# Kernel tuning notes

Measured on AMD Instinct MI355X. Metric: run time of the kernel, lower is better.

## Reference

```python
import jax, jax.numpy as jnp
import numpy as np

B, S, D, H = 4, 2048, 1024, 16
DH = D // H


def setup_inputs() -> dict:
    key = jax.random.key(0)
    ks = jax.random.split(key, 12)
    scale = 1.0 / np.sqrt(D)
    inp = {
        'q': jax.random.normal(ks[0], (B, S, D), jnp.float32),
        'k': jax.random.normal(ks[1], (B, S, D), jnp.float32),
        'v': jax.random.normal(ks[2], (B, S, D), jnp.float32),
        # causal mask, broadcast over batch and heads; masked where mask == 0
        'mask': jnp.tril(jnp.ones((S, S), jnp.int32))[None, None, :, :],
        'wq': jax.random.normal(ks[3], (D, D), jnp.float32) * scale,
        'bq': jnp.zeros((D,), jnp.float32),
        'wk': jax.random.normal(ks[4], (D, D), jnp.float32) * scale,
        'bk': jnp.zeros((D,), jnp.float32),
        'wv': jax.random.normal(ks[5], (D, D), jnp.float32) * scale,
        'bv': jnp.zeros((D,), jnp.float32),
        'wo': jax.random.normal(ks[6], (D, D), jnp.float32) * scale,
        'bo': jnp.zeros((D,), jnp.float32),
    }
    return inp


def _split_heads(x):
    # [B, S, D] -> [B, H, S, DH]
    b, s, _ = x.shape
    return x.reshape(b, s, H, DH).transpose(0, 2, 1, 3)


def reference(q, k, v, mask, wq, bq, wk, bk, wv, bv, wo, bo):
    # torch Linear: y = x @ W.T + b
    qh = _split_heads(q @ wq.T + bq)
    kh = _split_heads(k @ wk.T + bk)
    vh = _split_heads(v @ wv.T + bv)
    attn = jnp.einsum('bhqd,bhkd->bhqk', qh, kh) / np.sqrt(DH)
    attn = jnp.where(mask == 0, jnp.float32(-10000.0), attn)
    attn = jax.nn.softmax(attn, axis=-1)
    out = jnp.einsum('bhqk,bhkd->bhqd', attn, vh)
    out = out.transpose(0, 2, 1, 3).reshape(q.shape[0], q.shape[1], D)
    return out @ wo.T + bo
```

## Files before the change

kernel.cpp:

```cpp
#include <hip/hip_runtime.h>

typedef __attribute__((ext_vector_type(8))) short short8;
typedef __attribute__((ext_vector_type(4))) float f32x4;
typedef __attribute__((ext_vector_type(16))) float f32x16;
typedef __attribute__((ext_vector_type(4))) unsigned short ushort4v;
typedef __attribute__((ext_vector_type(8))) unsigned short ushort8v;
typedef __attribute__((ext_vector_type(4))) unsigned int uint4v;

#define S_LEN 2048
#define DMODEL 1024
#define NHEAD 16
#define DHEAD 64
#define BATCH 4
#define NEGBIG (-1.0e30f)
#define LOG2E 1.4426950408889634f

__device__ __forceinline__ unsigned short f2bf(float f) {
  unsigned int u = __builtin_bit_cast(unsigned int, f);
  u += 0x7fffu + ((u >> 16) & 1u);
  return (unsigned short)(u >> 16);
}

__device__ __forceinline__ void gload16(const void* src, void* lds_dst) {
  __builtin_amdgcn_global_load_lds(
      (const __attribute__((address_space(1))) unsigned int*)src,
      (__attribute__((address_space(3))) unsigned int*)lds_dst, 16, 0, 0);
}

__global__ __launch_bounds__(256) void cvt3_kernel(
    const float* __restrict__ i0, const float* __restrict__ i1, const float* __restrict__ i2,
    unsigned short* __restrict__ o0, unsigned short* __restrict__ o1,
    unsigned short* __restrict__ o2, int n) {
  const float* in = (blockIdx.y == 0) ? i0 : (blockIdx.y == 1) ? i1 : i2;
  unsigned short* out = (blockIdx.y == 0) ? o0 : (blockIdx.y == 1) ? o1 : o2;
  int idx = blockIdx.x * blockDim.x + threadIdx.x;
  int stride = gridDim.x * blockDim.x;
  for (int j = idx * 8; j < n; j += stride * 8) {
    float4 a = *(const float4*)(in + j);
    float4 b = *(const float4*)(in + j + 4);
    ushort8v r;
    r[0] = f2bf(a.x); r[1] = f2bf(a.y); r[2] = f2bf(a.z); r[3] = f2bf(a.w);
    r[4] = f2bf(b.x); r[5] = f2bf(b.y); r[6] = f2bf(b.z); r[7] = f2bf(b.w);
    *(ushort8v*)(out + j) = r;
  }
}

__global__ __launch_bounds__(256) void cvt4_kernel(
    const float* __restrict__ i0, const float* __restrict__ i1,
    const float* __restrict__ i2, const float* __restrict__ i3,
    unsigned short* __restrict__ o0, unsigned short* __restrict__ o1,
    unsigned short* __restrict__ o2, unsigned short* __restrict__ o3, int n) {
  const float* in = (blockIdx.y == 0) ? i0 : (blockIdx.y == 1) ? i1 : (blockIdx.y == 2) ? i2 : i3;
  unsigned short* out = (blockIdx.y == 0) ? o0 : (blockIdx.y == 1) ? o1 : (blockIdx.y == 2) ? o2 : o3;
  int idx = blockIdx.x * blockDim.x + threadIdx.x;
  int stride = gridDim.x * blockDim.x;
  for (int j = idx * 8; j < n; j += stride * 8) {
    float4 a = *(const float4*)(in + j);
    float4 b = *(const float4*)(in + j + 4);
    ushort8v r;
    r[0] = f2bf(a.x); r[1] = f2bf(a.y); r[2] = f2bf(a.z); r[3] = f2bf(a.w);
    r[4] = f2bf(b.x); r[5] = f2bf(b.y); r[6] = f2bf(b.z); r[7] = f2bf(b.w);
    *(ushort8v*)(out + j) = r;
  }
}

template <int MODE>
__global__ __launch_bounds__(256) void gemm_kernel(
    const unsigned short* __restrict__ A, const unsigned short* __restrict__ W,
    const float* __restrict__ bias, void* __restrict__ outp, int M, int N, int K,
    float oscale) {
  __shared__ char lds[32768];
  const int tid = threadIdx.x;
  const int lane = tid & 63;
  const int wv = tid >> 6;
  const int wr = wv >> 1, wc = wv & 1;
  const int l16 = lane & 15, lg = lane >> 4;

  const int nbx = N >> 7;
  const int nwg = gridDim.x;
  const int swz = (blockIdx.x & 7) * (nwg >> 3) + (blockIdx.x >> 3);
  const int tm = swz / nbx, tn = swz % nbx;

  const char* Ab = (const char*)A;
  const char* Wb = (const char*)W;

  f32x4 acc[4][4] = {};

  for (int k0 = 0; k0 < K; k0 += 64) {
#pragma unroll
    for (int i = 0; i < 8; ++i) {
      int ch = wv * 8 + i;
      int chl = ch & 15;
      int r = chl * 8 + (lane >> 3);
      int cb = ((lane & 7) * 16) ^ ((r & 7) << 4);
      const char* src = (ch < 16)
          ? Ab + ((size_t)(tm * 128 + r) * K + k0) * 2 + cb
          : Wb + ((size_t)(tn * 128 + r) * K + k0) * 2 + cb;
      gload16(src, lds + ch * 1024);
    }
    __syncthreads();
#pragma unroll
    for (int ks = 0; ks < 2; ++ks) {
      const int cbase = (ks * 32 + lg * 8) * 2;
      short8 af[4], bfr[4];
#pragma unroll
      for (int m = 0; m < 4; ++m) {
        int r = wr * 64 + m * 16 + l16;
        af[m] = *(const short8*)(lds + r * 128 + (cbase ^ ((r & 7) << 4)));
      }
#pragma unroll
      for (int n = 0; n < 4; ++n) {
        int r = wc * 64 + n * 16 + l16;
        bfr[n] = *(const short8*)(lds + 16384 + r * 128 + (cbase ^ ((r & 7) << 4)));
      }
#pragma unroll
      for (int m = 0; m < 4; ++m)
#pragma unroll
        for (int n = 0; n < 4; ++n)
          acc[m][n] = __builtin_amdgcn_mfma_f32_16x16x32_bf16(af[m], bfr[n], acc[m][n], 0, 0, 0);
    }
    __syncthreads();
  }

#pragma unroll
  for (int n = 0; n < 4; ++n) {
    int gn = tn * 128 + wc * 64 + n * 16 + l16;
    float bv = bias[gn];
#pragma unroll
    for (int m = 0; m < 4; ++m) {
      int gm0 = tm * 128 + wr * 64 + m * 16 + lg * 4;
      f32x4 a = acc[m][n];
      if (MODE == 2) {
        float* of = (float*)outp;
#pragma unroll
        for (int rr = 0; rr < 4; ++rr)
          of[(size_t)(gm0 + rr) * N + gn] = (a[rr] + bv) * oscale;
      } else if (MODE == 0) {
        unsigned short* ou = (unsigned short*)outp;
        int h = gn >> 6, dh = gn & 63;
#pragma unroll
        for (int rr = 0; rr < 4; ++rr) {
          int gm = gm0 + rr;
          int b = gm >> 11, s = gm & 2047;
          ou[(((size_t)b * NHEAD + h) * S_LEN + s) * DHEAD + dh] = f2bf((a[rr] + bv) * oscale);
        }
      } else {
        unsigned short* ou = (unsigned short*)outp;
        int h = gn >> 6, dh = gn & 63;
        int b = gm0 >> 11, s0 = gm0 & 2047;
        ushort4v pk;
        pk[0] = f2bf((a[0] + bv) * oscale); pk[1] = f2bf((a[1] + bv) * oscale);
        pk[2] = f2bf((a[2] + bv) * oscale); pk[3] = f2bf((a[3] + bv) * oscale);
        *(ushort4v*)(ou + (((size_t)b * NHEAD + h) * DHEAD + dh) * S_LEN + s0) = pk;
      }
    }
  }
}

__global__ __launch_bounds__(256) void attn_kernel(
    const unsigned short* __restrict__ qh, const unsigned short* __restrict__ kh,
    const unsigned short* __restrict__ vt, unsigned short* __restrict__ aout) {
  __shared__ char lds[32768];
  const int tid = threadIdx.x;
  const int lane = tid & 63;
  const int w = tid >> 6;
  const int l31 = lane & 31;
  const int l5 = lane >> 5;
  const int bh = blockIdx.y;
  const int b = bh >> 4, h = bh & 15;

  const char* kbase = (const char*)(kh + (size_t)bh * S_LEN * DHEAD);
  const char* vbase = (const char*)(vt + (size_t)bh * S_LEN * DHEAD);
  const unsigned short* qbase = qh + (size_t)bh * S_LEN * DHEAD;

  const int la = lane >> 3, lb = lane & 7;

  for (int ph = 0; ph < 2; ++ph) {
    const int qb = ph ? (15 - (int)blockIdx.x) : (int)blockIdx.x;
    const int q0 = qb * 128;
    const int wq0 = q0 + w * 32;
    const int qg = wq0 + l31;
    const int nt = qb * 2 + 2;

    short8 qf[4];
#pragma unroll
    for (int f = 0; f < 4; ++f)
      qf[f] = *(const short8*)(qbase + (size_t)qg * DHEAD + f * 16 + l5 * 8);

    f32x16 oa[2] = {};
    float mrun = NEGBIG, lr = 0.f;

#pragma unroll
    for (int i = 0; i < 2; ++i) {
      int ch = w * 2 + i;
      int r = ch * 8 + la;
      int cb = (lb * 16) ^ ((r & 7) << 4);
      gload16(kbase + (size_t)r * 128 + cb, lds + ch * 1024 + lane * 16);
      gload16(vbase + (size_t)r * 4096 + cb, lds + 8192 + ch * 1024 + lane * 16);
    }
    __syncthreads();
    int cur = 0;

    for (int t = 0; t < nt; ++t) {
      const int kv0 = t * 64;
      if (t + 1 < nt) {
        char* nb = lds + (cur ^ 1) * 16384;
#pragma unroll
        for (int i = 0; i < 2; ++i) {
          int ch = w * 2 + i;
          int r = ch * 8 + la;
          int cb = (lb * 16) ^ ((r & 7) << 4);
          gload16(kbase + (size_t)(kv0 + 64 + r) * 128 + cb, nb + ch * 1024 + lane * 16);
          gload16(vbase + (size_t)r * 4096 + (size_t)(kv0 + 64) * 2 + cb,
                  nb + 8192 + ch * 1024 + lane * 16);
        }
      }
      if (kv0 <= wq0 + 31) {
        const char* ldk = lds + cur * 16384;
        const char* ldv = ldk + 8192;

        f32x16 sa[2] = {};
#pragma unroll
        for (int kb2 = 0; kb2 < 2; ++kb2) {
          const int kr = kb2 * 32 + l31;
          const char* rowp = ldk + kr * 128;
          const int sw = (kr & 7) << 4;
#pragma unroll
          for (int f = 0; f < 4; ++f) {
            short8 kf = *(const short8*)(rowp + ((f * 32 + l5 * 16) ^ sw));
            sa[kb2] = __builtin_amdgcn_mfma_f32_32x32x16_bf16(kf, qf[f], sa[kb2], 0, 0, 0);
          }
        }

        if (kv0 + 63 > wq0) {
#pragma unroll
          for (int kb2 = 0; kb2 < 2; ++kb2)
#pragma unroll
            for (int r = 0; r < 16; ++r) {
              int kgl = kv0 + kb2 * 32 + (r & 3) + 8 * (r >> 2) + 4 * l5;
              if (kgl > qg) sa[kb2][r] = NEGBIG;
            }
        }

        float pm = sa[0][0];
#pragma unroll
        for (int kb2 = 0; kb2 < 2; ++kb2)
#pragma unroll
          for (int r = 0; r < 16; ++r) pm = fmaxf(pm, sa[kb2][r]);
        pm = fmaxf(pm, __shfl_xor(pm, 32));

        if (!__all(pm <= mrun + 8.f)) {
          float mN = fmaxf(mrun, pm);
          float sc = __builtin_amdgcn_exp2f(mrun - mN);
          mrun = mN;
          lr *= sc;
          oa[0] *= sc;
          oa[1] *= sc;
        }

        float rs = 0.f;
        short8 pfrag[4];
#pragma unroll
        for (int kb2 = 0; kb2 < 2; ++kb2) {
          unsigned int wpk[8];
#pragma unroll
          for (int i = 0; i < 8; ++i) {
            float p0 = __builtin_amdgcn_exp2f(sa[kb2][2 * i] - mrun);
            float p1 = __builtin_amdgcn_exp2f(sa[kb2][2 * i + 1] - mrun);
            rs += p0 + p1;
            wpk[i] = (unsigned int)f2bf(p0) | ((unsigned int)f2bf(p1) << 16);
          }
#pragma unroll
          for (int g = 0; g < 2; ++g) {
            unsigned int o0 = l5 ? wpk[4 * g + 2] : wpk[4 * g];
            unsigned int o1 = l5 ? wpk[4 * g + 3] : wpk[4 * g + 1];
            unsigned int s0 = l5 ? wpk[4 * g] : wpk[4 * g + 2];
            unsigned int s1 = l5 ? wpk[4 * g + 1] : wpk[4 * g + 3];
            unsigned int r0 = (unsigned int)__shfl_xor((int)s0, 32);
            unsigned int r1 = (unsigned int)__shfl_xor((int)s1, 32);
            uint4v fw;
            fw[0] = l5 ? r0 : o0;
            fw[1] = l5 ? r1 : o1;
            fw[2] = l5 ? o0 : r0;
            fw[3] = l5 ? o1 : r1;
            pfrag[kb2 * 2 + g] = __builtin_bit_cast(short8, fw);
          }
        }
        rs += __shfl_xor(rs, 32);
        lr += rs;

#pragma unroll
        for (int db = 0; db < 2; ++db) {
          const int vr = db * 32 + l31;
          const char* rowp = ldv + vr * 128;
          const int sw = (vr & 7) << 4;
#pragma unroll
          for (int f = 0; f < 4; ++f) {
            short8 vf = *(const short8*)(rowp + ((f * 32 + l5 * 16) ^ sw));
            oa[db] = __builtin_amdgcn_mfma_f32_32x32x16_bf16(vf, pfrag[f], oa[db], 0, 0, 0);
          }
        }
      }
      __syncthreads();
      cur ^= 1;
    }

    float rl = 1.0f / lr;
    unsigned short* obase = aout + ((size_t)(b * S_LEN + qg)) * DMODEL + h * DHEAD;
#pragma unroll
    for (int db = 0; db < 2; ++db)
#pragma unroll
      for (int rq = 0; rq < 4; ++rq) {
        ushort4v pk;
#pragma unroll
        for (int j = 0; j < 4; ++j)
          pk[j] = f2bf(oa[db][rq * 4 + j] * rl);
        *(ushort4v*)(obase + db * 32 + 8 * rq + 4 * l5) = pk;
      }
  }
}

extern "C" void kernel_launch(void* const* d_in, const int* in_sizes, int n_in,
                              void* d_out, int out_size, void* d_ws, size_t ws_size,
                              hipStream_t stream) {
  (void)in_sizes; (void)n_in; (void)out_size; (void)ws_size;
  const float* q  = (const float*)d_in[0];
  const float* k  = (const float*)d_in[1];
  const float* v  = (const float*)d_in[2];
  const float* wq = (const float*)d_in[4];
  const float* bq = (const float*)d_in[5];
  const float* wk = (const float*)d_in[6];
  const float* bk = (const float*)d_in[7];
  const float* wv = (const float*)d_in[8];
  const float* bv = (const float*)d_in[9];
  const float* wo = (const float*)d_in[10];
  const float* bo = (const float*)d_in[11];

  const size_t NACT = (size_t)BATCH * S_LEN * DMODEL;
  const size_t NW = (size_t)DMODEL * DMODEL;
  unsigned short* qb  = (unsigned short*)d_ws;
  unsigned short* kb  = qb + NACT;
  unsigned short* vb  = kb + NACT;
  unsigned short* wqb = vb + NACT;
  unsigned short* wkb = wqb + NW;
  unsigned short* wvb = wkb + NW;
  unsigned short* wob = wvb + NW;
  unsigned short* qhb = wob + NW;
  unsigned short* khb = qhb + NACT;
  unsigned short* vtb = khb + NACT;
  unsigned short* aout = qb;

  dim3 blk(256);
  cvt3_kernel<<<dim3(2048, 3), blk, 0, stream>>>(q, k, v, qb, kb, vb, (int)NACT);
  cvt4_kernel<<<dim3(512, 4), blk, 0, stream>>>(wq, wk, wv, wo, wqb, wkb, wvb, wob, (int)NW);

  const int M = BATCH * S_LEN, N = DMODEL, K = DMODEL;
  const int grid = (M / 128) * (N / 128);
  gemm_kernel<0><<<grid, blk, 0, stream>>>(qb, wqb, bq, qhb, M, N, K, 0.125f * LOG2E);
  gemm_kernel<0><<<grid, blk, 0, stream>>>(kb, wkb, bk, khb, M, N, K, 1.0f);
  gemm_kernel<1><<<grid, blk, 0, stream>>>(vb, wvb, bv, vtb, M, N, K, 1.0f);

  attn_kernel<<<dim3(8, 64), blk, 0, stream>>>(qhb, khb, vtb, aout);

  gemm_kernel<2><<<grid, blk, 0, stream>>>(aout, wob, bo, d_out, M, N, K, 1.0f);
}
```

Baseline: 204.3 us.

## Use 512-thread attention blocks covering 256 queries instead of paired 128-query phases

The attention kernel now launches 8 waves per block, each block handling a 256-query tile in a single pass, and drops the two-phase pairing of a short and a long causal tile. Each thread issues one K and one V async load per KV tile, so more waves share each LDS-staged tile. Blocks are ordered with the heaviest query tiles first. This trades the old per-block causal load balancing for better K/V reuse and fewer loop phases, and risks tail imbalance between blocks with very different tile counts.

```diff
diff --git a/kernel.cpp b/kernel.cpp
--- a/kernel.cpp
+++ b/kernel.cpp
@@ -157,7 +157,7 @@
   }
 }
 
-__global__ __launch_bounds__(256) void attn_kernel(
+__global__ __launch_bounds__(512) void attn_kernel(
     const unsigned short* __restrict__ qh, const unsigned short* __restrict__ kh,
     const unsigned short* __restrict__ vt, unsigned short* __restrict__ aout) {
   __shared__ char lds[32768];
@@ -173,151 +173,138 @@
   const char* vbase = (const char*)(vt + (size_t)bh * S_LEN * DHEAD);
   const unsigned short* qbase = qh + (size_t)bh * S_LEN * DHEAD;
 
-  const int la = lane >> 3, lb = lane & 7;
-
-  for (int ph = 0; ph < 2; ++ph) {
-    const int qb = ph ? (15 - (int)blockIdx.x) : (int)blockIdx.x;
-    const int q0 = qb * 128;
-    const int wq0 = q0 + w * 32;
-    const int qg = wq0 + l31;
-    const int nt = qb * 2 + 2;
-
-    short8 qf[4];
-#pragma unroll
-    for (int f = 0; f < 4; ++f)
-      qf[f] = *(const short8*)(qbase + (size_t)qg * DHEAD + f * 16 + l5 * 8);
-
-    f32x16 oa[2] = {};
-    float mrun = NEGBIG, lr = 0.f;
-
-#pragma unroll
-    for (int i = 0; i < 2; ++i) {
-      int ch = w * 2 + i;
-      int r = ch * 8 + la;
-      int cb = (lb * 16) ^ ((r & 7) << 4);
-      gload16(kbase + (size_t)r * 128 + cb, lds + ch * 1024 + lane * 16);
-      gload16(vbase + (size_t)r * 4096 + cb, lds + 8192 + ch * 1024 + lane * 16);
+  const int sr = tid >> 3;
+  const int scb = ((tid & 7) * 16) ^ ((sr & 7) << 4);
+  const int sdst = tid * 16;
+
+  const int qb = 7 - (int)blockIdx.x;
+  const int q0 = qb * 256;
+  const int wq0 = q0 + w * 32;
+  const int qg = wq0 + l31;
+  const int nt = qb * 4 + 4;
+
+  short8 qf[4];
+#pragma unroll
+  for (int f = 0; f < 4; ++f)
+    qf[f] = *(const short8*)(qbase + (size_t)qg * DHEAD + f * 16 + l5 * 8);
+
+  f32x16 oa[2] = {};
+  float mrun = NEGBIG, lr = 0.f;
+
+  gload16(kbase + (size_t)sr * 128 + scb, lds + sdst);
+  gload16(vbase + (size_t)sr * 4096 + scb, lds + 8192 + sdst);
+  __syncthreads();
+  int cur = 0;
+
+  for (int t = 0; t < nt; ++t) {
+    const int kv0 = t * 64;
+    if (t + 1 < nt) {
+      char* nb = lds + (cur ^ 1) * 16384;
+      gload16(kbase + (size_t)(kv0 + 64 + sr) * 128 + scb, nb + sdst);
+      gload16(vbase + (size_t)sr * 4096 + (size_t)(kv0 + 64) * 2 + scb, nb + 8192 + sdst);
+    }
+    if (kv0 <= wq0 + 31) {
+      const char* ldk = lds + cur * 16384;
+      const char* ldv = ldk + 8192;
+
+      f32x16 sa[2] = {};
+#pragma unroll
+      for (int kb2 = 0; kb2 < 2; ++kb2) {
+        const int kr = kb2 * 32 + l31;
+        const char* rowp = ldk + kr * 128;
+        const int sw = (kr & 7) << 4;
+#pragma unroll
+        for (int f = 0; f < 4; ++f) {
+          short8 kf = *(const short8*)(rowp + ((f * 32 + l5 * 16) ^ sw));
+          sa[kb2] = __builtin_amdgcn_mfma_f32_32x32x16_bf16(kf, qf[f], sa[kb2], 0, 0, 0);
+        }
+      }
+
+      if (kv0 + 63 > wq0) {
+#pragma unroll
+        for (int kb2 = 0; kb2 < 2; ++kb2)
+#pragma unroll
+          for (int r = 0; r < 16; ++r) {
+            int kgl = kv0 + kb2 * 32 + (r & 3) + 8 * (r >> 2) + 4 * l5;
+            if (kgl > qg) sa[kb2][r] = NEGBIG;
+          }
+      }
+
+      float pm = sa[0][0];
+#pragma unroll
+      for (int kb2 = 0; kb2 < 2; ++kb2)
+#pragma unroll
+        for (int r = 0; r < 16; ++r) pm = fmaxf(pm, sa[kb2][r]);
+      pm = fmaxf(pm, __shfl_xor(pm, 32));
+
+      if (!__all(pm <= mrun + 8.f)) {
+        float mN = fmaxf(mrun, pm);
+        float sc = __builtin_amdgcn_exp2f(mrun - mN);
+        mrun = mN;
+        lr *= sc;
+        oa[0] *= sc;
+        oa[1] *= sc;
+      }
+
+      float rs = 0.f;
+      short8 pfrag[4];
+#pragma unroll
+      for (int kb2 = 0; kb2 < 2; ++kb2) {
+        unsigned int wpk[8];
+#pragma unroll
+        for (int i = 0; i < 8; ++i) {
+          float p0 = __builtin_amdgcn_exp2f(sa[kb2][2 * i] - mrun);
+          float p1 = __builtin_amdgcn_exp2f(sa[kb2][2 * i + 1] - mrun);
+          rs += p0 + p1;
+          wpk[i] = (unsigned int)f2bf(p0) | ((unsigned int)f2bf(p1) << 16);
+        }
+#pragma unroll
+        for (int g = 0; g < 2; ++g) {
+          unsigned int o0 = l5 ? wpk[4 * g + 2] : wpk[4 * g];
+          unsigned int o1 = l5 ? wpk[4 * g + 3] : wpk[4 * g + 1];
+          unsigned int s0 = l5 ? wpk[4 * g] : wpk[4 * g + 2];
+          unsigned int s1 = l5 ? wpk[4 * g + 1] : wpk[4 * g + 3];
+          unsigned int r0 = (unsigned int)__shfl_xor((int)s0, 32);
+          unsigned int r1 = (unsigned int)__shfl_xor((int)s1, 32);
+          uint4v fw;
+          fw[0] = l5 ? r0 : o0;
+          fw[1] = l5 ? r1 : o1;
+          fw[2] = l5 ? o0 : r0;
+          fw[3] = l5 ? o1 : r1;
+          pfrag[kb2 * 2 + g] = __builtin_bit_cast(short8, fw);
+        }
+      }
+      rs += __shfl_xor(rs, 32);
+      lr += rs;
+
+#pragma unroll
+      for (int db = 0; db < 2; ++db) {
+        const int vr = db * 32 + l31;
+        const char* rowp = ldv + vr * 128;
+        const int sw = (vr & 7) << 4;
+#pragma unroll
+        for (int f = 0; f < 4; ++f) {
+          short8 vf = *(const short8*)(rowp + ((f * 32 + l5 * 16) ^ sw));
+          oa[db] = __builtin_amdgcn_mfma_f32_32x32x16_bf16(vf, pfrag[f], oa[db], 0, 0, 0);
+        }
+      }
     }
     __syncthreads();
-    int cur = 0;
-
-    for (int t = 0; t < nt; ++t) {
-      const int kv0 = t * 64;
-      if (t + 1 < nt) {
-        char* nb = lds + (cur ^ 1) * 16384;
-#pragma unroll
-        for (int i = 0; i < 2; ++i) {
-          int ch = w * 2 + i;
-          int r = ch * 8 + la;
-          int cb = (lb * 16) ^ ((r & 7) << 4);
-          gload16(kbase + (size_t)(kv0 + 64 + r) * 128 + cb, nb + ch * 1024 + lane * 16);
-          gload16(vbase + (size_t)r * 4096 + (size_t)(kv0 + 64) * 2 + cb,
-                  nb + 8192 + ch * 1024 + lane * 16);
-        }
-      }
-      if (kv0 <= wq0 + 31) {
-        const char* ldk = lds + cur * 16384;
-        const char* ldv = ldk + 8192;
-
-        f32x16 sa[2] = {};
-#pragma unroll
-        for (int kb2 = 0; kb2 < 2; ++kb2) {
-          const int kr = kb2 * 32 + l31;
-          const char* rowp = ldk + kr * 128;
-          const int sw = (kr & 7) << 4;
-#pragma unroll
-          for (int f = 0; f < 4; ++f) {
-            short8 kf = *(const short8*)(rowp + ((f * 32 + l5 * 16) ^ sw));
-            sa[kb2] = __builtin_amdgcn_mfma_f32_32x32x16_bf16(kf, qf[f], sa[kb2], 0, 0, 0);
-          }
-        }
-
-        if (kv0 + 63 > wq0) {
-#pragma unroll
-          for (int kb2 = 0; kb2 < 2; ++kb2)
-#pragma unroll
-            for (int r = 0; r < 16; ++r) {
-              int kgl = kv0 + kb2 * 32 + (r & 3) + 8 * (r >> 2) + 4 * l5;
-              if (kgl > qg) sa[kb2][r] = NEGBIG;
-            }
-        }
-
-        float pm = sa[0][0];
-#pragma unroll
-        for (int kb2 = 0; kb2 < 2; ++kb2)
-#pragma unroll
-          for (int r = 0; r < 16; ++r) pm = fmaxf(pm, sa[kb2][r]);
-        pm = fmaxf(pm, __shfl_xor(pm, 32));
-
-        if (!__all(pm <= mrun + 8.f)) {
-          float mN = fmaxf(mrun, pm);
-          float sc = __builtin_amdgcn_exp2f(mrun - mN);
-          mrun = mN;
-          lr *= sc;
-          oa[0] *= sc;
-          oa[1] *= sc;
-        }
-
-        float rs = 0.f;
-        short8 pfrag[4];
-#pragma unroll
-        for (int kb2 = 0; kb2 < 2; ++kb2) {
-          unsigned int wpk[8];
-#pragma unroll
-          for (int i = 0; i < 8; ++i) {
-            float p0 = __builtin_amdgcn_exp2f(sa[kb2][2 * i] - mrun);
-            float p1 = __builtin_amdgcn_exp2f(sa[kb2][2 * i + 1] - mrun);
-            rs += p0 + p1;
-            wpk[i] = (unsigned int)f2bf(p0) | ((unsigned int)f2bf(p1) << 16);
-          }
-#pragma unroll
-          for (int g = 0; g < 2; ++g) {
-            unsigned int o0 = l5 ? wpk[4 * g + 2] : wpk[4 * g];
-            unsigned int o1 = l5 ? wpk[4 * g + 3] : wpk[4 * g + 1];
-            unsigned int s0 = l5 ? wpk[4 * g] : wpk[4 * g + 2];
-            unsigned int s1 = l5 ? wpk[4 * g + 1] : wpk[4 * g + 3];
-            unsigned int r0 = (unsigned int)__shfl_xor((int)s0, 32);
-            unsigned int r1 = (unsigned int)__shfl_xor((int)s1, 32);
-            uint4v fw;
-            fw[0] = l5 ? r0 : o0;
-            fw[1] = l5 ? r1 : o1;
-            fw[2] = l5 ? o0 : r0;
-            fw[3] = l5 ? o1 : r1;
-            pfrag[kb2 * 2 + g] = __builtin_bit_cast(short8, fw);
-          }
-        }
-        rs += __shfl_xor(rs, 32);
-        lr += rs;
-
-#pragma unroll
-        for (int db = 0; db < 2; ++db) {
-          const int vr = db * 32 + l31;
-          const char* rowp = ldv + vr * 128;
-          const int sw = (vr & 7) << 4;
-#pragma unroll
-          for (int f = 0; f < 4; ++f) {
-            short8 vf = *(const short8*)(rowp + ((f * 32 + l5 * 16) ^ sw));
-            oa[db] = __builtin_amdgcn_mfma_f32_32x32x16_bf16(vf, pfrag[f], oa[db], 0, 0, 0);
-          }
-        }
-      }
-      __syncthreads();
-      cur ^= 1;
-    }
-
-    float rl = 1.0f / lr;
-    unsigned short* obase = aout + ((size_t)(b * S_LEN + qg)) * DMODEL + h * DHEAD;
-#pragma unroll
-    for (int db = 0; db < 2; ++db)
-#pragma unroll
-      for (int rq = 0; rq < 4; ++rq) {
-        ushort4v pk;
-#pragma unroll
-        for (int j = 0; j < 4; ++j)
-          pk[j] = f2bf(oa[db][rq * 4 + j] * rl);
-        *(ushort4v*)(obase + db * 32 + 8 * rq + 4 * l5) = pk;
-      }
-  }
+    cur ^= 1;
+  }
+
+  float rl = 1.0f / lr;
+  unsigned short* obase = aout + ((size_t)(b * S_LEN + qg)) * DMODEL + h * DHEAD;
+#pragma unroll
+  for (int db = 0; db < 2; ++db)
+#pragma unroll
+    for (int rq = 0; rq < 4; ++rq) {
+      ushort4v pk;
+#pragma unroll
+      for (int j = 0; j < 4; ++j)
+        pk[j] = f2bf(oa[db][rq * 4 + j] * rl);
+      *(ushort4v*)(obase + db * 32 + 8 * rq + 4 * l5) = pk;
+    }
 }
 
 extern "C" void kernel_launch(void* const* d_in, const int* in_sizes, int n_in,
@@ -360,7 +347,7 @@
   gemm_kernel<0><<<grid, blk, 0, stream>>>(kb, wkb, bk, khb, M, N, K, 1.0f);
   gemm_kernel<1><<<grid, blk, 0, stream>>>(vb, wvb, bv, vtb, M, N, K, 1.0f);
 
-  attn_kernel<<<dim3(8, 64), blk, 0, stream>>>(qhb, khb, vtb, aout);
+  attn_kernel<<<dim3(8, 64), dim3(512), 0, stream>>>(qhb, khb, vtb, aout);
 
   gemm_kernel<2><<<grid, blk, 0, stream>>>(aout, wob, bo, d_out, M, N, K, 1.0f);
 }
```

Measured after the change: 235.4 us. 1.15x slower.

## Triple-buffer K/V tiles in attention with vmcnt-based partial waits

Applied to the files above, without the earlier changes.

Moves the attention kernel from double to triple buffering of K/V tiles in LDS, prefetching two tiles ahead. Full __syncthreads is replaced by s_waitcnt vmcnt(4) plus a raw barrier, so the next tile's loads can stay in flight across iterations. It also reorganises the row-max reduction into four independent chains for more ILP. In exchange LDS use rises to 48KB, which can lower occupancy. Out-of-range tiles issue dummy loads from row 0, and a vmcnt(0) wait is added at the end of each phase.

```diff
diff --git a/kernel.cpp b/kernel.cpp
--- a/kernel.cpp
+++ b/kernel.cpp
@@ -160,7 +160,7 @@
 __global__ __launch_bounds__(256) void attn_kernel(
     const unsigned short* __restrict__ qh, const unsigned short* __restrict__ kh,
     const unsigned short* __restrict__ vt, unsigned short* __restrict__ aout) {
-  __shared__ char lds[32768];
+  __shared__ char lds[49152];
   const int tid = threadIdx.x;
   const int lane = tid & 63;
   const int w = tid >> 6;
@@ -190,33 +190,32 @@
     f32x16 oa[2] = {};
     float mrun = NEGBIG, lr = 0.f;
 
-#pragma unroll
-    for (int i = 0; i < 2; ++i) {
-      int ch = w * 2 + i;
-      int r = ch * 8 + la;
-      int cb = (lb * 16) ^ ((r & 7) << 4);
-      gload16(kbase + (size_t)r * 128 + cb, lds + ch * 1024 + lane * 16);
-      gload16(vbase + (size_t)r * 4096 + cb, lds + 8192 + ch * 1024 + lane * 16);
-    }
-    __syncthreads();
-    int cur = 0;
-
+    auto issue = [&](int tt, int buf) {
+      const int kvr = (tt < nt) ? tt * 64 : 0;
+      char* nb = lds + buf * 16384;
+#pragma unroll
+      for (int i = 0; i < 2; ++i) {
+        int ch = w * 2 + i;
+        int r = ch * 8 + la;
+        int cb = (lb * 16) ^ ((r & 7) << 4);
+        gload16(kbase + (size_t)(kvr + r) * 128 + cb, nb + ch * 1024 + lane * 16);
+        gload16(vbase + (size_t)r * 4096 + (size_t)kvr * 2 + cb,
+                nb + 8192 + ch * 1024 + lane * 16);
+      }
+    };
+
+    issue(0, 0);
+    issue(1, 1);
+    asm volatile("s_waitcnt vmcnt(4)" ::: "memory");
+    __builtin_amdgcn_s_barrier();
+    asm volatile("" ::: "memory");
+
+    int b0 = 0, b1 = 1, b2 = 2;
     for (int t = 0; t < nt; ++t) {
       const int kv0 = t * 64;
-      if (t + 1 < nt) {
-        char* nb = lds + (cur ^ 1) * 16384;
-#pragma unroll
-        for (int i = 0; i < 2; ++i) {
-          int ch = w * 2 + i;
-          int r = ch * 8 + la;
-          int cb = (lb * 16) ^ ((r & 7) << 4);
-          gload16(kbase + (size_t)(kv0 + 64 + r) * 128 + cb, nb + ch * 1024 + lane * 16);
-          gload16(vbase + (size_t)r * 4096 + (size_t)(kv0 + 64) * 2 + cb,
-                  nb + 8192 + ch * 1024 + lane * 16);
-        }
-      }
+      issue(t + 2, b2);
       if (kv0 <= wq0 + 31) {
-        const char* ldk = lds + cur * 16384;
+        const char* ldk = lds + b0 * 16384;
         const char* ldv = ldk + 8192;
 
         f32x16 sa[2] = {};
@@ -242,11 +241,15 @@
             }
         }
 
-        float pm = sa[0][0];
-#pragma unroll
-        for (int kb2 = 0; kb2 < 2; ++kb2)
-#pragma unroll
-          for (int r = 0; r < 16; ++r) pm = fmaxf(pm, sa[kb2][r]);
+        float m4[4];
+#pragma unroll
+        for (int j = 0; j < 4; ++j) m4[j] = fmaxf(sa[0][j], sa[1][j]);
+#pragma unroll
+        for (int i = 1; i < 4; ++i)
+#pragma unroll
+          for (int j = 0; j < 4; ++j)
+            m4[j] = fmaxf(m4[j], fmaxf(sa[0][4 * i + j], sa[1][4 * i + j]));
+        float pm = fmaxf(fmaxf(m4[0], m4[1]), fmaxf(m4[2], m4[3]));
         pm = fmaxf(pm, __shfl_xor(pm, 32));
 
         if (!__all(pm <= mrun + 8.f)) {
@@ -301,8 +304,10 @@
           }
         }
       }
-      __syncthreads();
-      cur ^= 1;
+      asm volatile("s_waitcnt vmcnt(4)" ::: "memory");
+      __builtin_amdgcn_s_barrier();
+      asm volatile("" ::: "memory");
+      int tmp = b0; b0 = b1; b1 = b2; b2 = tmp;
     }
 
     float rl = 1.0f / lr;
@@ -317,6 +322,10 @@
           pk[j] = f2bf(oa[db][rq * 4 + j] * rl);
         *(ushort4v*)(obase + db * 32 + 8 * rq + 4 * l5) = pk;
       }
+
+    asm volatile("s_waitcnt vmcnt(0)" ::: "memory");
+    __builtin_amdgcn_s_barrier();
+    asm volatile("" ::: "memory");
   }
 }
 
```

Result: slower. 209.7 us (+2.6%).

## Fuse fp32-to-bf16 activation conversion into a batched QKV GEMM and reschedule attention

Applied to the files above, without the earlier changes.

Drops the separate activation conversion kernel. The three Q/K/V projections become one launch with a z-dimension, and each of those GEMMs loads fp32 activations into registers, converts them to bf16 and writes them to LDS, with a register prefetch of the next K-slab. The attention kernel stops pairing a light and a heavy query block in one workgroup and launches one workgroup per query block, heavy blocks first, with heads on the x dimension. This removes the extra read and write of the bf16 activation copies and two launches, but A-tile loads now go through registers instead of direct-to-LDS loads, and the attention work is less balanced per workgroup.

```diff
diff --git a/kernel.cpp b/kernel.cpp
--- a/kernel.cpp
+++ b/kernel.cpp
@@ -25,24 +25,6 @@
   __builtin_amdgcn_global_load_lds(
       (const __attribute__((address_space(1))) unsigned int*)src,
       (__attribute__((address_space(3))) unsigned int*)lds_dst, 16, 0, 0);
-}
-
-__global__ __launch_bounds__(256) void cvt3_kernel(
-    const float* __restrict__ i0, const float* __restrict__ i1, const float* __restrict__ i2,
-    unsigned short* __restrict__ o0, unsigned short* __restrict__ o1,
-    unsigned short* __restrict__ o2, int n) {
-  const float* in = (blockIdx.y == 0) ? i0 : (blockIdx.y == 1) ? i1 : i2;
-  unsigned short* out = (blockIdx.y == 0) ? o0 : (blockIdx.y == 1) ? o1 : o2;
-  int idx = blockIdx.x * blockDim.x + threadIdx.x;
-  int stride = gridDim.x * blockDim.x;
-  for (int j = idx * 8; j < n; j += stride * 8) {
-    float4 a = *(const float4*)(in + j);
-    float4 b = *(const float4*)(in + j + 4);
-    ushort8v r;
-    r[0] = f2bf(a.x); r[1] = f2bf(a.y); r[2] = f2bf(a.z); r[3] = f2bf(a.w);
-    r[4] = f2bf(b.x); r[5] = f2bf(b.y); r[6] = f2bf(b.z); r[7] = f2bf(b.w);
-    *(ushort8v*)(out + j) = r;
-  }
 }
 
 __global__ __launch_bounds__(256) void cvt4_kernel(
@@ -64,11 +46,127 @@
   }
 }
 
-template <int MODE>
-__global__ __launch_bounds__(256) void gemm_kernel(
+__global__ __launch_bounds__(256) void qkv_gemm_kernel(
+    const float* __restrict__ Aq, const float* __restrict__ Ak, const float* __restrict__ Av,
+    const unsigned short* __restrict__ Wq, const unsigned short* __restrict__ Wk,
+    const unsigned short* __restrict__ Wv,
+    const float* __restrict__ bq, const float* __restrict__ bk, const float* __restrict__ bv,
+    unsigned short* __restrict__ oq, unsigned short* __restrict__ ok,
+    unsigned short* __restrict__ ov) {
+  const int z = blockIdx.z;
+  const float* A = (z == 0) ? Aq : (z == 1) ? Ak : Av;
+  const unsigned short* W = (z == 0) ? Wq : (z == 1) ? Wk : Wv;
+  const float* bias = (z == 0) ? bq : (z == 1) ? bk : bv;
+  unsigned short* out = (z == 0) ? oq : (z == 1) ? ok : ov;
+  const float oscale = (z == 0) ? 0.125f * LOG2E : 1.0f;
+  const int N = DMODEL, K = DMODEL;
+
+  __shared__ char lds[32768];
+  const int tid = threadIdx.x;
+  const int lane = tid & 63;
+  const int wv = tid >> 6;
+  const int wr = wv >> 1, wc = wv & 1;
+  const int l16 = lane & 15, lg = lane >> 4;
+
+  const int nbx = N >> 7;
+  const int swz = (blockIdx.x & 7) * ((int)gridDim.x >> 3) + (blockIdx.x >> 3);
+  const int tm = swz / nbx, tn = swz % nbx;
+
+  const char* Wb = (const char*)W;
+
+  const int arow[4] = {(tid >> 3), 32 + (tid >> 3), 64 + (tid >> 3), 96 + (tid >> 3)};
+  const int aslot = tid & 7;
+
+  float4 areg[4][2];
+#pragma unroll
+  for (int j = 0; j < 4; ++j) {
+    const float* ap = A + (size_t)(tm * 128 + arow[j]) * K + aslot * 8;
+    areg[j][0] = *(const float4*)ap;
+    areg[j][1] = *(const float4*)(ap + 4);
+  }
+
+  f32x4 acc[4][4] = {};
+
+  for (int k0 = 0; k0 < K; k0 += 64) {
+#pragma unroll
+    for (int i = 0; i < 4; ++i) {
+      int ch = wv * 4 + i;
+      int r = ch * 8 + (lane >> 3);
+      int cb = ((lane & 7) * 16) ^ ((r & 7) << 4);
+      gload16(Wb + ((size_t)(tn * 128 + r) * K + k0) * 2 + cb, lds + 16384 + ch * 1024);
+    }
+#pragma unroll
+    for (int j = 0; j < 4; ++j) {
+      ushort8v w8;
+      w8[0] = f2bf(areg[j][0].x); w8[1] = f2bf(areg[j][0].y);
+      w8[2] = f2bf(areg[j][0].z); w8[3] = f2bf(areg[j][0].w);
+      w8[4] = f2bf(areg[j][1].x); w8[5] = f2bf(areg[j][1].y);
+      w8[6] = f2bf(areg[j][1].z); w8[7] = f2bf(areg[j][1].w);
+      int r = arow[j];
+      *(ushort8v*)(lds + r * 128 + ((aslot * 16) ^ ((r & 7) << 4))) = w8;
+    }
+    if (k0 + 64 < K) {
+#pragma unroll
+      for (int j = 0; j < 4; ++j) {
+        const float* ap = A + (size_t)(tm * 128 + arow[j]) * K + (k0 + 64) + aslot * 8;
+        areg[j][0] = *(const float4*)ap;
+        areg[j][1] = *(const float4*)(ap + 4);
+      }
+    }
+    __syncthreads();
+#pragma unroll
+    for (int ks = 0; ks < 2; ++ks) {
+      const int cbase = (ks * 32 + lg * 8) * 2;
+      short8 af[4], bfr[4];
+#pragma unroll
+      for (int m = 0; m < 4; ++m) {
+        int r = wr * 64 + m * 16 + l16;
+        af[m] = *(const short8*)(lds + r * 128 + (cbase ^ ((r & 7) << 4)));
+      }
+#pragma unroll
+      for (int n = 0; n < 4; ++n) {
+        int r = wc * 64 + n * 16 + l16;
+        bfr[n] = *(const short8*)(lds + 16384 + r * 128 + (cbase ^ ((r & 7) << 4)));
+      }
+#pragma unroll
+      for (int m = 0; m < 4; ++m)
+#pragma unroll
+        for (int n = 0; n < 4; ++n)
+          acc[m][n] = __builtin_amdgcn_mfma_f32_16x16x32_bf16(af[m], bfr[n], acc[m][n], 0, 0, 0);
+    }
+    __syncthreads();
+  }
+
+#pragma unroll
+  for (int n = 0; n < 4; ++n) {
+    int gn = tn * 128 + wc * 64 + n * 16 + l16;
+    float bv2 = bias[gn];
+    int h = gn >> 6, dh = gn & 63;
+#pragma unroll
+    for (int m = 0; m < 4; ++m) {
+      int gm0 = tm * 128 + wr * 64 + m * 16 + lg * 4;
+      f32x4 a = acc[m][n];
+      if (z < 2) {
+#pragma unroll
+        for (int rr = 0; rr < 4; ++rr) {
+          int gm = gm0 + rr;
+          int b = gm >> 11, s = gm & 2047;
+          out[(((size_t)b * NHEAD + h) * S_LEN + s) * DHEAD + dh] = f2bf((a[rr] + bv2) * oscale);
+        }
+      } else {
+        int b = gm0 >> 11, s0 = gm0 & 2047;
+        ushort4v pk;
+        pk[0] = f2bf(a[0] + bv2); pk[1] = f2bf(a[1] + bv2);
+        pk[2] = f2bf(a[2] + bv2); pk[3] = f2bf(a[3] + bv2);
+        *(ushort4v*)(out + (((size_t)b * NHEAD + h) * DHEAD + dh) * S_LEN + s0) = pk;
+      }
+    }
+  }
+}
+
+__global__ __launch_bounds__(256) void gemm_o_kernel(
     const unsigned short* __restrict__ A, const unsigned short* __restrict__ W,
-    const float* __restrict__ bias, void* __restrict__ outp, int M, int N, int K,
-    float oscale) {
+    const float* __restrict__ bias, float* __restrict__ outp, int M, int N, int K) {
   __shared__ char lds[32768];
   const int tid = threadIdx.x;
   const int lane = tid & 63;
@@ -130,29 +228,9 @@
     for (int m = 0; m < 4; ++m) {
       int gm0 = tm * 128 + wr * 64 + m * 16 + lg * 4;
       f32x4 a = acc[m][n];
-      if (MODE == 2) {
-        float* of = (float*)outp;
-#pragma unroll
-        for (int rr = 0; rr < 4; ++rr)
-          of[(size_t)(gm0 + rr) * N + gn] = (a[rr] + bv) * oscale;
-      } else if (MODE == 0) {
-        unsigned short* ou = (unsigned short*)outp;
-        int h = gn >> 6, dh = gn & 63;
-#pragma unroll
-        for (int rr = 0; rr < 4; ++rr) {
-          int gm = gm0 + rr;
-          int b = gm >> 11, s = gm & 2047;
-          ou[(((size_t)b * NHEAD + h) * S_LEN + s) * DHEAD + dh] = f2bf((a[rr] + bv) * oscale);
-        }
-      } else {
-        unsigned short* ou = (unsigned short*)outp;
-        int h = gn >> 6, dh = gn & 63;
-        int b = gm0 >> 11, s0 = gm0 & 2047;
-        ushort4v pk;
-        pk[0] = f2bf((a[0] + bv) * oscale); pk[1] = f2bf((a[1] + bv) * oscale);
-        pk[2] = f2bf((a[2] + bv) * oscale); pk[3] = f2bf((a[3] + bv) * oscale);
-        *(ushort4v*)(ou + (((size_t)b * NHEAD + h) * DHEAD + dh) * S_LEN + s0) = pk;
-      }
+#pragma unroll
+      for (int rr = 0; rr < 4; ++rr)
+        outp[(size_t)(gm0 + rr) * N + gn] = a[rr] + bv;
     }
   }
 }
@@ -166,7 +244,7 @@
   const int w = tid >> 6;
   const int l31 = lane & 31;
   const int l5 = lane >> 5;
-  const int bh = blockIdx.y;
+  const int bh = blockIdx.x;
   const int b = bh >> 4, h = bh & 15;
 
   const char* kbase = (const char*)(kh + (size_t)bh * S_LEN * DHEAD);
@@ -175,149 +253,147 @@
 
   const int la = lane >> 3, lb = lane & 7;
 
-  for (int ph = 0; ph < 2; ++ph) {
-    const int qb = ph ? (15 - (int)blockIdx.x) : (int)blockIdx.x;
-    const int q0 = qb * 128;
-    const int wq0 = q0 + w * 32;
-    const int qg = wq0 + l31;
-    const int nt = qb * 2 + 2;
-
-    short8 qf[4];
-#pragma unroll
-    for (int f = 0; f < 4; ++f)
-      qf[f] = *(const short8*)(qbase + (size_t)qg * DHEAD + f * 16 + l5 * 8);
-
-    f32x16 oa[2] = {};
-    float mrun = NEGBIG, lr = 0.f;
-
-#pragma unroll
-    for (int i = 0; i < 2; ++i) {
-      int ch = w * 2 + i;
-      int r = ch * 8 + la;
-      int cb = (lb * 16) ^ ((r & 7) << 4);
-      gload16(kbase + (size_t)r * 128 + cb, lds + ch * 1024 + lane * 16);
-      gload16(vbase + (size_t)r * 4096 + cb, lds + 8192 + ch * 1024 + lane * 16);
+  const int qb = 15 - (int)blockIdx.y;
+  const int q0 = qb * 128;
+  const int wq0 = q0 + w * 32;
+  const int qg = wq0 + l31;
+  const int nt = qb * 2 + 2;
+
+  short8 qf[4];
+#pragma unroll
+  for (int f = 0; f < 4; ++f)
+    qf[f] = *(const short8*)(qbase + (size_t)qg * DHEAD + f * 16 + l5 * 8);
+
+  f32x16 oa[2] = {};
+  float mrun = NEGBIG, lr = 0.f;
+
+#pragma unroll
+  for (int i = 0; i < 2; ++i) {
+    int ch = w * 2 + i;
+    int r = ch * 8 + la;
+    int cb = (lb * 16) ^ ((r & 7) << 4);
+    gload16(kbase + (size_t)r * 128 + cb, lds + ch * 1024 + lane * 16);
+    gload16(vbase + (size_t)r * 4096 + cb, lds + 8192 + ch * 1024 + lane * 16);
+  }
+  __syncthreads();
+  int cur = 0;
+
+  for (int t = 0; t < nt; ++t) {
+    const int kv0 = t * 64;
+    if (t + 1 < nt) {
+      char* nb = lds + (cur ^ 1) * 16384;
+#pragma unroll
+      for (int i = 0; i < 2; ++i) {
+        int ch = w * 2 + i;
+        int r = ch * 8 + la;
+        int cb = (lb * 16) ^ ((r & 7) << 4);
+        gload16(kbase + (size_t)(kv0 + 64 + r) * 128 + cb, nb + ch * 1024 + lane * 16);
+        gload16(vbase + (size_t)r * 4096 + (size_t)(kv0 + 64) * 2 + cb,
+                nb + 8192 + ch * 1024 + lane * 16);
+      }
+    }
+    if (kv0 <= wq0 + 31) {
+      const char* ldk = lds + cur * 16384;
+      const char* ldv = ldk + 8192;
+
+      f32x16 sa[2] = {};
+#pragma unroll
+      for (int kb2 = 0; kb2 < 2; ++kb2) {
+        const int kr = kb2 * 32 + l31;
+        const char* rowp = ldk + kr * 128;
+        const int sw = (kr & 7) << 4;
+#pragma unroll
+        for (int f = 0; f < 4; ++f) {
+          short8 kf = *(const short8*)(rowp + ((f * 32 + l5 * 16) ^ sw));
+          sa[kb2] = __builtin_amdgcn_mfma_f32_32x32x16_bf16(kf, qf[f], sa[kb2], 0, 0, 0);
+        }
+      }
+
+      if (kv0 + 63 > wq0) {
+#pragma unroll
+        for (int kb2 = 0; kb2 < 2; ++kb2)
+#pragma unroll
+          for (int r = 0; r < 16; ++r) {
+            int kgl = kv0 + kb2 * 32 + (r & 3) + 8 * (r >> 2) + 4 * l5;
+            if (kgl > qg) sa[kb2][r] = NEGBIG;
+          }
+      }
+
+      float pm = sa[0][0];
+#pragma unroll
+      for (int kb2 = 0; kb2 < 2; ++kb2)
+#pragma unroll
+        for (int r = 0; r < 16; ++r) pm = fmaxf(pm, sa[kb2][r]);
+      pm = fmaxf(pm, __shfl_xor(pm, 32));
+
+      if (!__all(pm <= mrun + 8.f)) {
+        float mN = fmaxf(mrun, pm);
+        float sc = __builtin_amdgcn_exp2f(mrun - mN);
+        mrun = mN;
+        lr *= sc;
+        oa[0] *= sc;
+        oa[1] *= sc;
+      }
+
+      float rs = 0.f;
+      short8 pfrag[4];
+#pragma unroll
+      for (int kb2 = 0; kb2 < 2; ++kb2) {
+        unsigned int wpk[8];
+#pragma unroll
+        for (int i = 0; i < 8; ++i) {
+          float p0 = __builtin_amdgcn_exp2f(sa[kb2][2 * i] - mrun);
+          float p1 = __builtin_amdgcn_exp2f(sa[kb2][2 * i + 1] - mrun);
+          rs += p0 + p1;
+          wpk[i] = (unsigned int)f2bf(p0) | ((unsigned int)f2bf(p1) << 16);
+        }
+#pragma unroll
+        for (int g = 0; g < 2; ++g) {
+          unsigned int o0 = l5 ? wpk[4 * g + 2] : wpk[4 * g];
+          unsigned int o1 = l5 ? wpk[4 * g + 3] : wpk[4 * g + 1];
+          unsigned int s0 = l5 ? wpk[4 * g] : wpk[4 * g + 2];
+          unsigned int s1 = l5 ? wpk[4 * g + 1] : wpk[4 * g + 3];
+          unsigned int r0 = (unsigned int)__shfl_xor((int)s0, 32);
+          unsigned int r1 = (unsigned int)__shfl_xor((int)s1, 32);
+          uint4v fw;
+          fw[0] = l5 ? r0 : o0;
+          fw[1] = l5 ? r1 : o1;
+          fw[2] = l5 ? o0 : r0;
+          fw[3] = l5 ? o1 : r1;
+          pfrag[kb2 * 2 + g] = __builtin_bit_cast(short8, fw);
+        }
+      }
+      rs += __shfl_xor(rs, 32);
+      lr += rs;
+
+#pragma unroll
+      for (int db = 0; db < 2; ++db) {
+        const int vr = db * 32 + l31;
+        const char* rowp = ldv + vr * 128;
+        const int sw = (vr & 7) << 4;
+#pragma unroll
+        for (int f = 0; f < 4; ++f) {
+          short8 vf = *(const short8*)(rowp + ((f * 32 + l5 * 16) ^ sw));
+          oa[db] = __builtin_amdgcn_mfma_f32_32x32x16_bf16(vf, pfrag[f], oa[db], 0, 0, 0);
+        }
+      }
     }
     __syncthreads();
-    int cur = 0;
-
-    for (int t = 0; t < nt; ++t) {
-      const int kv0 = t * 64;
-      if (t + 1 < nt) {
-        char* nb = lds + (cur ^ 1) * 16384;
-#pragma unroll
-        for (int i = 0; i < 2; ++i) {
-          int ch = w * 2 + i;
-          int r = ch * 8 + la;
-          int cb = (lb * 16) ^ ((r & 7) << 4);
-          gload16(kbase + (size_t)(kv0 + 64 + r) * 128 + cb, nb + ch * 1024 + lane * 16);
-          gload16(vbase + (size_t)r * 4096 + (size_t)(kv0 + 64) * 2 + cb,
-                  nb + 8192 + ch * 1024 + lane * 16);
-        }
-      }
-      if (kv0 <= wq0 + 31) {
-        const char* ldk = lds + cur * 16384;
-        const char* ldv = ldk + 8192;
-
-        f32x16 sa[2] = {};
-#pragma unroll
-        for (int kb2 = 0; kb2 < 2; ++kb2) {
-          const int kr = kb2 * 32 + l31;
-          const char* rowp = ldk + kr * 128;
-          const int sw = (kr & 7) << 4;
-#pragma unroll
-          for (int f = 0; f < 4; ++f) {
-            short8 kf = *(const short8*)(rowp + ((f * 32 + l5 * 16) ^ sw));
-            sa[kb2] = __builtin_amdgcn_mfma_f32_32x32x16_bf16(kf, qf[f], sa[kb2], 0, 0, 0);
-          }
-        }
-
-        if (kv0 + 63 > wq0) {
-#pragma unroll
-          for (int kb2 = 0; kb2 < 2; ++kb2)
-#pragma unroll
-            for (int r = 0; r < 16; ++r) {
-              int kgl = kv0 + kb2 * 32 + (r & 3) + 8 * (r >> 2) + 4 * l5;
-              if (kgl > qg) sa[kb2][r] = NEGBIG;
-            }
-        }
-
-        float pm = sa[0][0];
-#pragma unroll
-        for (int kb2 = 0; kb2 < 2; ++kb2)
-#pragma unroll
-          for (int r = 0; r < 16; ++r) pm = fmaxf(pm, sa[kb2][r]);
-        pm = fmaxf(pm, __shfl_xor(pm, 32));
-
-        if (!__all(pm <= mrun + 8.f)) {
-          float mN = fmaxf(mrun, pm);
-          float sc = __builtin_amdgcn_exp2f(mrun - mN);
-          mrun = mN;
-          lr *= sc;
-          oa[0] *= sc;
-          oa[1] *= sc;
-        }
-
-        float rs = 0.f;
-        short8 pfrag[4];
-#pragma unroll
-        for (int kb2 = 0; kb2 < 2; ++kb2) {
-          unsigned int wpk[8];
-#pragma unroll
-          for (int i = 0; i < 8; ++i) {
-            float p0 = __builtin_amdgcn_exp2f(sa[kb2][2 * i] - mrun);
-            float p1 = __builtin_amdgcn_exp2f(sa[kb2][2 * i + 1] - mrun);
-            rs += p0 + p1;
-            wpk[i] = (unsigned int)f2bf(p0) | ((unsigned int)f2bf(p1) << 16);
-          }
-#pragma unroll
-          for (int g = 0; g < 2; ++g) {
-            unsigned int o0 = l5 ? wpk[4 * g + 2] : wpk[4 * g];
-            unsigned int o1 = l5 ? wpk[4 * g + 3] : wpk[4 * g + 1];
-            unsigned int s0 = l5 ? wpk[4 * g] : wpk[4 * g + 2];
-            unsigned int s1 = l5 ? wpk[4 * g + 1] : wpk[4 * g + 3];
-            unsigned int r0 = (unsigned int)__shfl_xor((int)s0, 32);
-            unsigned int r1 = (unsigned int)__shfl_xor((int)s1, 32);
-            uint4v fw;
-            fw[0] = l5 ? r0 : o0;
-            fw[1] = l5 ? r1 : o1;
-            fw[2] = l5 ? o0 : r0;
-            fw[3] = l5 ? o1 : r1;
-            pfrag[kb2 * 2 + g] = __builtin_bit_cast(short8, fw);
-          }
-        }
-        rs += __shfl_xor(rs, 32);
-        lr += rs;
-
-#pragma unroll
-        for (int db = 0; db < 2; ++db) {
-          const int vr = db * 32 + l31;
-          const char* rowp = ldv + vr * 128;
-          const int sw = (vr & 7) << 4;
-#pragma unroll
-          for (int f = 0; f < 4; ++f) {
-            short8 vf = *(const short8*)(rowp + ((f * 32 + l5 * 16) ^ sw));
-            oa[db] = __builtin_amdgcn_mfma_f32_32x32x16_bf16(vf, pfrag[f], oa[db], 0, 0, 0);
-          }
-        }
-      }
-      __syncthreads();
-      cur ^= 1;
-    }
-
-    float rl = 1.0f / lr;
-    unsigned short* obase = aout + ((size_t)(b * S_LEN + qg)) * DMODEL + h * DHEAD;
-#pragma unroll
-    for (int db = 0; db < 2; ++db)
-#pragma unroll
-      for (int rq = 0; rq < 4; ++rq) {
-        ushort4v pk;
-#pragma unroll
-        for (int j = 0; j < 4; ++j)
-          pk[j] = f2bf(oa[db][rq * 4 + j] * rl);
-        *(ushort4v*)(obase + db * 32 + 8 * rq + 4 * l5) = pk;
-      }
-  }
+    cur ^= 1;
+  }
+
+  float rl = 1.0f / lr;
+  unsigned short* obase = aout + ((size_t)(b * S_LEN + qg)) * DMODEL + h * DHEAD;
+#pragma unroll
+  for (int db = 0; db < 2; ++db)
+#pragma unroll
+    for (int rq = 0; rq < 4; ++rq) {
+      ushort4v pk;
+#pragma unroll
+      for (int j = 0; j < 4; ++j)
+        pk[j] = f2bf(oa[db][rq * 4 + j] * rl);
+      *(ushort4v*)(obase + db * 32 + 8 * rq + 4 * l5) = pk;
+    }
 }
 
 extern "C" void kernel_launch(void* const* d_in, const int* in_sizes, int n_in,
@@ -338,29 +414,24 @@
 
   const size_t NACT = (size_t)BATCH * S_LEN * DMODEL;
   const size_t NW = (size_t)DMODEL * DMODEL;
-  unsigned short* qb  = (unsigned short*)d_ws;
-  unsigned short* kb  = qb + NACT;
-  unsigned short* vb  = kb + NACT;
-  unsigned short* wqb = vb + NACT;
+  unsigned short* wqb = (unsigned short*)d_ws;
   unsigned short* wkb = wqb + NW;
   unsigned short* wvb = wkb + NW;
   unsigned short* wob = wvb + NW;
   unsigned short* qhb = wob + NW;
   unsigned short* khb = qhb + NACT;
   unsigned short* vtb = khb + NACT;
-  unsigned short* aout = qb;
+  unsigned short* aout = vtb + NACT;
 
   dim3 blk(256);
-  cvt3_kernel<<<dim3(2048, 3), blk, 0, stream>>>(q, k, v, qb, kb, vb, (int)NACT);
   cvt4_kernel<<<dim3(512, 4), blk, 0, stream>>>(wq, wk, wv, wo, wqb, wkb, wvb, wob, (int)NW);
 
   const int M = BATCH * S_LEN, N = DMODEL, K = DMODEL;
   const int grid = (M / 128) * (N / 128);
-  gemm_kernel<0><<<grid, blk, 0, stream>>>(qb, wqb, bq, qhb, M, N, K, 0.125f * LOG2E);
-  gemm_kernel<0><<<grid, blk, 0, stream>>>(kb, wkb, bk, khb, M, N, K, 1.0f);
-  gemm_kernel<1><<<grid, blk, 0, stream>>>(vb, wvb, bv, vtb, M, N, K, 1.0f);
-
-  attn_kernel<<<dim3(8, 64), blk, 0, stream>>>(qhb, khb, vtb, aout);
-
-  gemm_kernel<2><<<grid, blk, 0, stream>>>(aout, wob, bo, d_out, M, N, K, 1.0f);
-}
+  qkv_gemm_kernel<<<dim3(grid, 1, 3), blk, 0, stream>>>(
+      q, k, v, wqb, wkb, wvb, bq, bk, bv, qhb, khb, vtb);
+
+  attn_kernel<<<dim3(64, 16), blk, 0, stream>>>(qhb, khb, vtb, aout);
+
+  gemm_o_kernel<<<grid, blk, 0, stream>>>(aout, wob, bo, (float*)d_out, M, N, K);
+}
```

After: 191.3 us. 6.4% less time.
